# Performance work log

Hardware: AMD Instinct MI355X
Metric: run time of the kernel (lower is better)

The kernel has to match this reference:

```python
import jax, jax.numpy as jnp
import numpy as np
from jax import lax

WS = 7            # window size
DIM = 256         # out_dim
HEADS = 8
HD = DIM // HEADS # head dim = 32
HIDDEN = 4 * DIM  # mlp hidden = 1024
IN_DIM = 512
EPS = 1e-6

def _rel_pos_index(ws):
    coords = np.stack(np.meshgrid(np.arange(ws), np.arange(ws), indexing='ij'))
    cf = coords.reshape(2, -1)
    rc = (cf[:, :, None] - cf[:, None, :]).transpose(1, 2, 0)
    rc[:, :, 0] += ws - 1
    rc[:, :, 1] += ws - 1
    rc[:, :, 0] *= 2 * ws - 1
    return rc.sum(-1)  # (N, N)

RPI = jnp.asarray(_rel_pos_index(WS))  # (49, 49) int

def _layernorm(x, g, b):
    m = jnp.mean(x, axis=-1, keepdims=True)
    v = jnp.mean(jnp.square(x - m), axis=-1, keepdims=True)
    return (x - m) * lax.rsqrt(v + EPS) * g + b

def setup_inputs() -> dict:
    key = jax.random.key(0)
    ks = jax.random.split(key, 16)
    s = 0.02
    inp = {
        'x': jax.random.normal(ks[0], (8, IN_DIM, 48, 48), jnp.float32),
        'skip_feat': jax.random.normal(ks[1], (8, DIM, 96, 96), jnp.float32),
        # ConvTranspose2d(in, out, k=2, s=2): weight (in, out, 2, 2), bias (out,)
        'up_w': jax.random.normal(ks[2], (IN_DIM, DIM, 2, 2), jnp.float32) * s,
        'up_b': jnp.zeros((DIM,), jnp.float32),
        # skip_adapter Conv2d(out, out, 1, bias=False)
        'skip_w': jax.random.normal(ks[3], (DIM, DIM, 1, 1), jnp.float32) * s,
        'gamma1': jnp.ones((DIM,), jnp.float32),
        'beta1': jnp.zeros((DIM,), jnp.float32),
        'qkv_w': jax.random.normal(ks[4], (3 * DIM, DIM), jnp.float32) * s,
        'qkv_b': jnp.zeros((3 * DIM,), jnp.float32),
        'rpb_table': jax.random.normal(ks[5], ((2 * WS - 1) ** 2, HEADS), jnp.float32) * s,
        'proj_w': jax.random.normal(ks[6], (DIM, DIM), jnp.float32) * s,
        'proj_b': jnp.zeros((DIM,), jnp.float32),
        'gamma2': jnp.ones((DIM,), jnp.float32),
        'beta2': jnp.zeros((DIM,), jnp.float32),
        'mlp_w1': jax.random.normal(ks[7], (HIDDEN, DIM), jnp.float32) * s,
        'mlp_b1': jnp.zeros((HIDDEN,), jnp.float32),
        'mlp_w2': jax.random.normal(ks[8], (DIM, HIDDEN), jnp.float32) * s,
        'mlp_b2': jnp.zeros((DIM,), jnp.float32),
    }
    return inp

def _forward(x, skip_feat, up_w, up_b, skip_w, gamma1, beta1, qkv_w, qkv_b,
             rpb_table, proj_w, proj_b, gamma2, beta2, mlp_w1, mlp_b1, mlp_w2, mlp_b2):
    B = x.shape[0]
    # ConvTranspose2d k=2 s=2 p=0 == lhs-dilated conv with spatially flipped kernel
    y = lax.conv_general_dilated(
        x, jnp.flip(up_w, (2, 3)), window_strides=(1, 1),
        padding=((1, 1), (1, 1)), lhs_dilation=(2, 2),
        dimension_numbers=('NCHW', 'IOHW', 'NCHW')) + up_b[None, :, None, None]
    shortcut = y  # (B, C, Hup, Wup)
    # skip adapter (1x1 conv, no bias); shapes match so no interpolate/adhoc conv
    y = y + jnp.einsum('oi,bihw->bohw', skip_w[:, :, 0, 0], skip_feat)
    xh = jnp.transpose(y, (0, 2, 3, 1))  # (B, H, W, C)
    H, W, C = xh.shape[1], xh.shape[2], xh.shape[3]
    xn = _layernorm(xh, gamma1, beta1)
    pad_b = (WS - H % WS) % WS
    pad_r = (WS - W % WS) % WS
    xp = jnp.pad(xn, ((0, 0), (0, pad_b), (0, pad_r), (0, 0)))
    Hp, Wp = H + pad_b, W + pad_r
    N = WS * WS
    # window partition -> (B * nWh * nWw, N, C)
    win = xp.reshape(B, Hp // WS, WS, Wp // WS, WS, C)
    win = jnp.transpose(win, (0, 1, 3, 2, 4, 5)).reshape(-1, N, C)
    B_ = win.shape[0]
    # attention
    qkv = (win @ qkv_w.T + qkv_b).reshape(B_, N, 3, HEADS, HD)
    qkv = jnp.transpose(qkv, (2, 0, 3, 1, 4))  # (3, B_, h, N, hd)
    q, k, v = qkv[0], qkv[1], qkv[2]
    attn = jnp.einsum('bhnd,bhmd->bhnm', q * (HD ** -0.5), k)
    bias = rpb_table[RPI.reshape(-1)].reshape(N, N, HEADS)
    attn = attn + jnp.transpose(bias, (2, 0, 1))[None]  # (B_, h, N, N)
    attn = jax.nn.softmax(attn, axis=-1)
    o = jnp.einsum('bhnm,bhmd->bhnd', attn, v)
    o = jnp.transpose(o, (0, 2, 1, 3)).reshape(B_, N, C)
    o = o @ proj_w.T + proj_b
    # window reverse + crop
    o = o.reshape(B, Hp // WS, Wp // WS, WS, WS, C)
    o = jnp.transpose(o, (0, 1, 3, 2, 4, 5)).reshape(B, Hp, Wp, C)[:, :H, :W]
    x2 = jnp.transpose(shortcut, (0, 2, 3, 1)) + o
    # MLP
    h = jax.nn.gelu(_layernorm(x2, gamma2, beta2) @ mlp_w1.T + mlp_b1, approximate=False)
    x3 = x2 + (h @ mlp_w2.T + mlp_b2)
    return jnp.transpose(x3, (0, 3, 1, 2))  # (B, C, Hup, Wup)

def reference(x, skip_feat, up_w, up_b, skip_w, gamma1, beta1, qkv_w, qkv_b,
              rpb_table, proj_w, proj_b, gamma2, beta2, mlp_w1, mlp_b1, mlp_w2, mlp_b2):
    return _forward(x, skip_feat, up_w, up_b, skip_w, gamma1, beta1, qkv_w, qkv_b,
                    rpb_table, proj_w, proj_b, gamma2, beta2, mlp_w1, mlp_b1, mlp_w2, mlp_b2)
```

## Files before the change

kernel.cpp:

```cpp
#include <hip/hip_runtime.h>

typedef __attribute__((ext_vector_type(8))) short short8;
typedef __attribute__((ext_vector_type(4))) float f32x4;
typedef __attribute__((ext_vector_type(4))) unsigned short u16x4;
typedef unsigned short u16;
typedef unsigned int u32;

#define DEV static __device__ __forceinline__

DEV u16 f2b(float f) {
  u32 u = __builtin_bit_cast(u32, f);
  return (u16)((u + 0x7fffu + ((u >> 16) & 1u)) >> 16);
}
DEV float b2f(u16 h) {
  u32 u = ((u32)h) << 16;
  return __builtin_bit_cast(float, u);
}
DEV short8 ld8(const u16* p) { return *reinterpret_cast<const short8*>(p); }
DEV f32x4 mfma16(short8 a, short8 b, f32x4 c) {
  return __builtin_amdgcn_mfma_f32_16x16x32_bf16(a, b, c, 0, 0, 0);
}
DEV float wredsum(float v) {
#pragma unroll
  for (int off = 1; off < 64; off <<= 1) v += __shfl_xor(v, off);
  return v;
}

#define GLL(gp, lp) __builtin_amdgcn_global_load_lds( \
    (const __attribute__((address_space(1))) void*)(gp), \
    (__attribute__((address_space(3))) void*)(lp), 16, 0, 0)

#define WQKV   0
#define WPROJ  196608
#define WM1    262144
#define WM2    524288
#define WSKIP  786432
#define WUP    851968

#define OFF_BIAS 2752512u
#define OFF_SC   2883584u
#define OFF_OVR  40632320u
#define OFF_STAT (OFF_OVR + 52000000u)
#define OFF_PST  (OFF_OVR + 52600000u)
#define OFF_SGB  (OFF_OVR + 55000000u)
#define WS_NEED  96227328u

__global__ void k_sentinel(float* out) { out[threadIdx.x] = 31337.0f; }

__global__ __launch_bounds__(256) void k_prep(
    const float* qkv_w, const float* proj_w, const float* mlp_w1,
    const float* mlp_w2, const float* skip_w, const float* up_w,
    const float* rpb, const float* g1, const float* g2, u16* W, float* bias_g) {
  int i = blockIdx.x * 256 + threadIdx.x;
  if (i < 196608) { W[WQKV + i] = f2b(qkv_w[i] * g1[i & 255]); return; }
  i -= 196608;
  if (i < 65536) { W[WPROJ + i] = f2b(proj_w[i]); return; }
  i -= 65536;
  if (i < 262144) { W[WM1 + i] = f2b(mlp_w1[i] * g2[i & 255]); return; }
  i -= 262144;
  if (i < 262144) { W[WM2 + i] = f2b(mlp_w2[i]); return; }
  i -= 262144;
  if (i < 65536) { W[WSKIP + i] = f2b(skip_w[i]); return; }
  i -= 65536;
  if (i < 524288) {
    int ci = i & 511; int rest = i >> 9; int co = rest & 255; int kk = rest >> 8;
    W[WUP + i] = f2b(up_w[ci * 1024 + co * 4 + kk]);
    return;
  }
  i -= 524288;
  if (i < 32768) {
    int h = i >> 12, r = i & 4095, ii = r >> 6, j = r & 63;
    float v;
    if (j >= 49) v = -1e30f;
    else if (ii >= 49) v = 0.f;
    else {
      int d0 = (ii / 7 - j / 7) + 6, d1 = (ii % 7 - j % 7) + 6;
      v = rpb[(d0 * 13 + d1) * 8 + h];
    }
    bias_g[i] = v;
  }
}

__global__ __launch_bounds__(256) void k_fold(
    const float* mlp_w1, const float* qkv_w, const float* g1, const float* be1,
    const float* g2, const float* be2, float* sgb) {
  int wave = threadIdx.x >> 6, lane = threadIdx.x & 63;
  int id = blockIdx.x * 4 + wave;
  const float* wsrc;
  const float* vec;
  int out;
  if (id < 1024) { wsrc = mlp_w1 + (size_t)id * 256; vec = g2; out = id; }
  else if (id < 2048) { wsrc = mlp_w1 + (size_t)(id - 1024) * 256; vec = be2; out = id; }
  else { wsrc = qkv_w + (size_t)(id - 2048) * 256; vec = be1; out = 2816 + (id - 2048); }
  float s = 0.f;
#pragma unroll
  for (int j = 0; j < 4; j++) {
    int k = j * 64 + lane;
    s += vec[k] * wsrc[k];
  }
  s = wredsum(s);
  if (lane == 0) sgb[out] = s;
}

__global__ __launch_bounds__(256) void k_tr(const float* src, u16* dst, int C, int HW) {
  __shared__ float t[32][33];
  int hw0 = blockIdx.x * 32, c0 = blockIdx.y * 32, b = blockIdx.z;
  int tx = threadIdx.x & 31, ty = threadIdx.x >> 5;
  const float* s = src + (size_t)b * C * HW;
  u16* d = dst + (size_t)b * C * HW;
#pragma unroll
  for (int i = 0; i < 4; i++)
    t[ty + i * 8][tx] = s[(size_t)(c0 + ty + i * 8) * HW + hw0 + tx];
  __syncthreads();
#pragma unroll
  for (int i = 0; i < 4; i++)
    d[(size_t)(hw0 + ty + i * 8) * C + c0 + tx] = f2b(t[tx][ty + i * 8]);
}

__global__ __launch_bounds__(256) void k_tr_skip(const float* src, u16* dst) {
  __shared__ float t[32][33];
  int w0 = blockIdx.x * 32, c0 = blockIdx.y * 32;
  int z = blockIdx.z;
  int b = z / 96, h = z - b * 96;
  int tx = threadIdx.x & 31, ty = threadIdx.x >> 5;
  const float* s = src + (size_t)b * 256 * 9216 + (size_t)h * 96;
  u16* d = dst + (((size_t)b * 96 + h) * 96) * 256;
#pragma unroll
  for (int i = 0; i < 4; i++)
    t[ty + i * 8][tx] = s[(size_t)(c0 + ty + i * 8) * 9216 + w0 + tx];
  __syncthreads();
#pragma unroll
  for (int i = 0; i < 4; i++)
    d[(size_t)(w0 + ty + i * 8) * 256 + c0 + tx] = f2b(t[tx][ty + i * 8]);
}

__global__ __launch_bounds__(256) void k1g(
    const u16* W, const u16* xt, const float* up_b, u16* sc) {
  __shared__ __align__(16) u16 Ab[2][4096];
  __shared__ __align__(16) u16 Bb[2][4096];
  int tid = threadIdx.x;
  int lane = tid & 63, wave = tid >> 6;
  int m = lane & 15, gq = lane >> 4;
  int wr = wave >> 1, wc = wave & 1;
  int bm = blockIdx.x * 128, bn = blockIdx.y * 128;
  int kk = blockIdx.z, kh = kk >> 1, kw = kk & 1;
  const u16* Ag = xt + (size_t)bm * 512;
  const u16* Bg = W + WUP + (size_t)kk * 131072 + (size_t)bn * 512;
  f32x4 acc[4][4] = {};
#pragma unroll
  for (int c = 0; c < 2; c++) {
    int flat = (wave * 2 + c) * 512 + lane * 8;
    int r = flat >> 5, cc = flat & 31;
    GLL(Ag + (size_t)r * 512 + cc, &Ab[0][(wave * 2 + c) * 512]);
    GLL(Bg + (size_t)r * 512 + cc, &Bb[0][(wave * 2 + c) * 512]);
  }
  __syncthreads();
  int cur = 0;
  for (int ki = 0; ki < 16; ki++) {
    if (ki < 15) {
      int kkk = (ki + 1) * 32;
#pragma unroll
      for (int c = 0; c < 2; c++) {
        int flat = (wave * 2 + c) * 512 + lane * 8;
        int r = flat >> 5, cc = flat & 31;
        GLL(Ag + (size_t)r * 512 + kkk + cc, &Ab[cur ^ 1][(wave * 2 + c) * 512]);
        GLL(Bg + (size_t)r * 512 + kkk + cc, &Bb[cur ^ 1][(wave * 2 + c) * 512]);
      }
    }
    short8 aF[4], bF[4];
#pragma unroll
    for (int mt = 0; mt < 4; mt++)
      aF[mt] = ld8(&Ab[cur][(wr * 64 + mt * 16 + m) * 32 + gq * 8]);
#pragma unroll
    for (int nt = 0; nt < 4; nt++)
      bF[nt] = ld8(&Bb[cur][(wc * 64 + nt * 16 + m) * 32 + gq * 8]);
#pragma unroll
    for (int mt = 0; mt < 4; mt++)
#pragma unroll
      for (int nt = 0; nt < 4; nt++)
        acc[mt][nt] = mfma16(aF[mt], bF[nt], acc[mt][nt]);
    __syncthreads();
    cur ^= 1;
  }
  float ub[4];
#pragma unroll
  for (int nt = 0; nt < 4; nt++) ub[nt] = up_b[bn + wc * 64 + nt * 16 + m];
#pragma unroll
  for (int mt = 0; mt < 4; mt++)
#pragma unroll
    for (int rr = 0; rr < 4; rr++) {
      int t = bm + wr * 64 + mt * 16 + gq * 4 + rr;
      int b = t / 2304, rem = t - b * 2304;
      int ih = rem / 48, iw = rem - ih * 48;
      int h = 2 * ih + kh, w = 2 * iw + kw;
      size_t tok = ((size_t)b * 96 + h) * 96 + w;
#pragma unroll
      for (int nt = 0; nt < 4; nt++) {
        int ch = bn + wc * 64 + nt * 16 + m;
        sc[tok * 256 + ch] = f2b(acc[mt][nt][rr] + ub[nt]);
      }
    }
}

__global__ __launch_bounds__(256) void k2y(
    const u16* W, const u16* skt, const u16* sc, u16* ybuf, float* pstat) {
  __shared__ __align__(16) u16 Ab[2][4096];
  __shared__ __align__(16) u16 Bb[2][4096];
  int tid = threadIdx.x;
  int lane = tid & 63, wave = tid >> 6;
  int m = lane & 15, gq = lane >> 4;
  int wr = wave >> 1, wc = wave & 1;
  int bm = blockIdx.x * 128, bn = blockIdx.y * 128;
  const u16* Ag = skt + (size_t)bm * 256;
  const u16* Bg = W + WSKIP + (size_t)bn * 256;
  f32x4 acc[4][4] = {};
#pragma unroll
  for (int c = 0; c < 2; c++) {
    int flat = (wave * 2 + c) * 512 + lane * 8;
    int r = flat >> 5, cc = flat & 31;
    GLL(Ag + (size_t)r * 256 + cc, &Ab[0][(wave * 2 + c) * 512]);
    GLL(Bg + (size_t)r * 256 + cc, &Bb[0][(wave * 2 + c) * 512]);
  }
  __syncthreads();
  int cur = 0;
  for (int ki = 0; ki < 8; ki++) {
    if (ki < 7) {
      int kk = (ki + 1) * 32;
#pragma unroll
      for (int c = 0; c < 2; c++) {
        int flat = (wave * 2 + c) * 512 + lane * 8;
        int r = flat >> 5, cc = flat & 31;
        GLL(Ag + (size_t)r * 256 + kk + cc, &Ab[cur ^ 1][(wave * 2 + c) * 512]);
        GLL(Bg + (size_t)r * 256 + kk + cc, &Bb[cur ^ 1][(wave * 2 + c) * 512]);
      }
    }
    short8 aF[4], bF[4];
#pragma unroll
    for (int mt = 0; mt < 4; mt++)
      aF[mt] = ld8(&Ab[cur][(wr * 64 + mt * 16 + m) * 32 + gq * 8]);
#pragma unroll
    for (int nt = 0; nt < 4; nt++)
      bF[nt] = ld8(&Bb[cur][(wc * 64 + nt * 16 + m) * 32 + gq * 8]);
#pragma unroll
    for (int mt = 0; mt < 4; mt++)
#pragma unroll
      for (int nt = 0; nt < 4; nt++)
        acc[mt][nt] = mfma16(aF[mt], bF[nt], acc[mt][nt]);
    __syncthreads();
    cur ^= 1;
  }
#pragma unroll
  for (int mt = 0; mt < 4; mt++)
#pragma unroll
    for (int rr = 0; rr < 4; rr++) {
      int tok = bm + wr * 64 + mt * 16 + gq * 4 + rr;
      float s = 0.f, s2 = 0.f;
#pragma unroll
      for (int nt = 0; nt < 4; nt++) {
        int ch = bn + wc * 64 + nt * 16 + m;
        float y = acc[mt][nt][rr] + b2f(sc[(size_t)tok * 256 + ch]);
        ybuf[(size_t)tok * 256 + ch] = f2b(y);
        s += y; s2 += y * y;
      }
#pragma unroll
      for (int off = 1; off < 16; off <<= 1) {
        s += __shfl_xor(s, off);
        s2 += __shfl_xor(s2, off);
      }
      if (m == 0) {
        int pi = (tok * 4 + blockIdx.y * 2 + wc) * 2;
        pstat[pi] = s;
        pstat[pi + 1] = s2;
      }
    }
}

__global__ __launch_bounds__(256) void k_statfin(const float* pstat, float* stat) {
  int row = blockIdx.x * 256 + threadIdx.x;
  float s = 0.f, s2 = 0.f;
#pragma unroll
  for (int j = 0; j < 4; j++) {
    s += pstat[(row * 4 + j) * 2];
    s2 += pstat[(row * 4 + j) * 2 + 1];
  }
  float mean = s * 0.00390625f;
  float var = s2 * 0.00390625f - mean * mean;
  float r = rsqrtf(var + 1e-6f);
  stat[row * 2] = r;
  stat[row * 2 + 1] = r * mean;
}

__global__ __launch_bounds__(256) void k23(
    const u16* W, const u16* ybuf, const float* stat, const float* sgb,
    const float* qkv_b, const float* bias_g, u16* obr) {
  __shared__ __align__(16) u16 yl[49 * 264];
  __shared__ __align__(16) u16 pws[4][6144];
  int tid = threadIdx.x;
  int lane = tid & 63, wave = tid >> 6;
  int m = lane & 15, gq = lane >> 4, k0 = gq * 8;
  int blk = blockIdx.x;
  int bimg = blk / 196, wl = blk - bimg * 196;
  int wrow = wl / 14, wcol = wl - wrow * 14;
  int h0 = wrow * 7, w0 = wcol * 7;
  u16* prv = pws[wave];
#pragma unroll
  for (int t = 0; t < 8; t++) {
    u16x4 z = {};
    *reinterpret_cast<u16x4*>(&prv[t * 256 + lane * 4]) = z;
  }
  for (int it = 0; it < 7; it++) {
    int flat = it * 256 + tid;
    if (flat < 1568) {
      int row = flat >> 5, cc = (flat & 31) * 8;
      int hh = h0 + row / 7, ww = w0 + row % 7;
      short8 v = {};
      if (hh < 96 && ww < 96) {
        int ras = (bimg * 96 + hh) * 96 + ww;
        short8 raw = ld8(ybuf + (size_t)ras * 256 + cc);
        float rs = stat[ras * 2], rmu = stat[ras * 2 + 1];
#pragma unroll
        for (int q2 = 0; q2 < 8; q2++) {
          float zz = b2f(((const u16*)&raw)[q2]) * rs - rmu;
          ((u16*)&v)[q2] = f2b(zz);
        }
      }
      *reinterpret_cast<short8*>(&yl[row * 264 + cc]) = v;
    }
  }
  __syncthreads();
  const float scale = 0.1767766952966369f;
#pragma unroll
  for (int hp = 0; hp < 2; hp++) {
    int h = wave * 2 + hp;
    {
      const u16* bb0 = W + WQKV + (size_t)(h * 32 + m) * 256;
      const u16* bb1 = W + WQKV + (size_t)(h * 32 + 16 + m) * 256;
      const u16* bb2 = W + WQKV + (size_t)(256 + h * 32 + m) * 256;
      const u16* bb3 = W + WQKV + (size_t)(256 + h * 32 + 16 + m) * 256;
      f32x4 acc[4][4] = {};
#pragma unroll 4
      for (int ks = 0; ks < 8; ks++) {
        short8 a[4];
#pragma unroll
        for (int mt = 0; mt < 4; mt++) {
          int row = mt * 16 + m; if (row > 48) row = 48;
          a[mt] = ld8(&yl[row * 264 + ks * 32 + k0]);
        }
        short8 b0 = ld8(bb0 + ks * 32 + k0);
        short8 b1 = ld8(bb1 + ks * 32 + k0);
        short8 b2 = ld8(bb2 + ks * 32 + k0);
        short8 b3 = ld8(bb3 + ks * 32 + k0);
#pragma unroll
        for (int mt = 0; mt < 4; mt++) {
          acc[mt][0] = mfma16(a[mt], b0, acc[mt][0]);
          acc[mt][1] = mfma16(a[mt], b1, acc[mt][1]);
          acc[mt][2] = mfma16(a[mt], b2, acc[mt][2]);
          acc[mt][3] = mfma16(a[mt], b3, acc[mt][3]);
        }
      }
#pragma unroll
      for (int nt = 0; nt < 4; nt++) {
        int hd = (nt & 1) * 16 + m;
        int c = (nt >> 1) * 256 + h * 32 + hd;
        float qb_ = qkv_b[c];
        float sb1 = sgb[2816 + c];
        int base = (nt < 2) ? 2048 : 3616;
#pragma unroll
        for (int mt = 0; mt < 4; mt++)
#pragma unroll
          for (int rr = 0; rr < 4; rr++) {
            int row = mt * 16 + gq * 4 + rr;
            if (row >= 49) continue;
            int hh = h0 + row / 7, ww = w0 + row % 7;
            float vf = (hh < 96 && ww < 96) ? 1.f : 0.f;
            prv[base + row * 32 + hd] = f2b(acc[mt][nt][rr] + vf * sb1 + qb_);
          }
      }
    }
    {
      const u16* bb0 = W + WQKV + (size_t)(512 + h * 32 + m) * 256;
      const u16* bb1 = W + WQKV + (size_t)(512 + h * 32 + 16 + m) * 256;
      f32x4 vacc[4][2] = {};
#pragma unroll 4
      for (int ks = 0; ks < 8; ks++) {
        short8 a[4];
#pragma unroll
        for (int mt = 0; mt < 4; mt++) {
          int row = mt * 16 + m; if (row > 48) row = 48;
          a[mt] = ld8(&yl[row * 264 + ks * 32 + k0]);
        }
        short8 b0 = ld8(bb0 + ks * 32 + k0);
        short8 b1 = ld8(bb1 + ks * 32 + k0);
#pragma unroll
        for (int mt = 0; mt < 4; mt++) {
          vacc[mt][0] = mfma16(a[mt], b0, vacc[mt][0]);
          vacc[mt][1] = mfma16(a[mt], b1, vacc[mt][1]);
        }
      }
      int vsw = (m & 7) * 8;
#pragma unroll
      for (int nv = 0; nv < 2; nv++) {
        int hd = nv * 16 + m;
        int c = 512 + h * 32 + hd;
        float qb_ = qkv_b[c];
        float sb1 = sgb[2816 + c];
#pragma unroll
        for (int mt = 0; mt < 4; mt++)
#pragma unroll
          for (int rr = 0; rr < 4; rr++) {
            int row = mt * 16 + gq * 4 + rr;
            if (row >= 49) continue;
            int hh = h0 + row / 7, ww = w0 + row % 7;
            float vf = (hh < 96 && ww < 96) ? 1.f : 0.f;
            prv[hd * 64 + (row ^ vsw)] = f2b(vacc[mt][nv][rr] + vf * sb1 + qb_);
          }
      }
    }
    short8 aq[4], bk[4];
#pragma unroll
    for (int mt = 0; mt < 4; mt++) { int i = mt * 16 + m; if (i > 48) i = 48; aq[mt] = ld8(&prv[2048 + i * 32 + k0]); }
#pragma unroll
    for (int nt = 0; nt < 4; nt++) { int j = nt * 16 + m; if (j > 48) j = 48; bk[nt] = ld8(&prv[3616 + j * 32 + k0]); }
    f32x4 s[4][4] = {};
#pragma unroll
    for (int mt = 0; mt < 4; mt++)
#pragma unroll
      for (int nt = 0; nt < 4; nt++)
        s[mt][nt] = mfma16(aq[mt], bk[nt], s[mt][nt]);
    const float* BI = bias_g + h * 4096;
    float rsum[4][4];
#pragma unroll
    for (int mt = 0; mt < 4; mt++)
#pragma unroll
      for (int rr = 0; rr < 4; rr++) {
        int i = mt * 16 + gq * 4 + rr;
        float sv[4];
        float mx = -1e38f;
#pragma unroll
        for (int nt = 0; nt < 4; nt++) {
          sv[nt] = s[mt][nt][rr] * scale + BI[i * 64 + nt * 16 + m];
          mx = fmaxf(mx, sv[nt]);
        }
        mx = fmaxf(mx, __shfl_xor(mx, 1));
        mx = fmaxf(mx, __shfl_xor(mx, 2));
        mx = fmaxf(mx, __shfl_xor(mx, 4));
        mx = fmaxf(mx, __shfl_xor(mx, 8));
        float sum = 0.f;
#pragma unroll
        for (int nt = 0; nt < 4; nt++) { sv[nt] = __expf(sv[nt] - mx); sum += sv[nt]; }
        sum += __shfl_xor(sum, 1);
        sum += __shfl_xor(sum, 2);
        sum += __shfl_xor(sum, 4);
        sum += __shfl_xor(sum, 8);
        rsum[mt][rr] = sum;
        int isw = (i & 7) * 8;
#pragma unroll
        for (int nt = 0; nt < 4; nt++) {
          int j = nt * 16 + m;
          prv[2048 + i * 64 + (j ^ isw)] = f2b(sv[nt]);
        }
      }
    f32x4 o[4][2] = {};
#pragma unroll
    for (int ks = 0; ks < 2; ks++) {
      short8 bv[2];
#pragma unroll
      for (int nt = 0; nt < 2; nt++) {
        int hd = nt * 16 + m;
        bv[nt] = ld8(&prv[hd * 64 + ((ks * 32 + k0) ^ ((hd & 7) * 8))]);
      }
#pragma unroll
      for (int mt = 0; mt < 4; mt++) {
        int i = mt * 16 + m;
        short8 ap = *reinterpret_cast<const short8*>(
            &prv[2048 + i * 64 + ((ks * 32 + k0) ^ ((i & 7) * 8))]);
#pragma unroll
        for (int nt = 0; nt < 2; nt++)
          o[mt][nt] = mfma16(ap, bv[nt], o[mt][nt]);
      }
    }
#pragma unroll
    for (int mt = 0; mt < 4; mt++)
#pragma unroll
      for (int rr = 0; rr < 4; rr++) {
        int i = mt * 16 + gq * 4 + rr;
        if (i >= 49) continue;
        int hh = h0 + i / 7, ww = w0 + i % 7;
        if (hh >= 96 || ww >= 96) continue;
        size_t ras = ((size_t)bimg * 96 + hh) * 96 + ww;
        float rinv = 1.f / rsum[mt][rr];
#pragma unroll
        for (int nt = 0; nt < 2; nt++) {
          int c = h * 32 + nt * 16 + m;
          obr[ras * 256 + c] = f2b(o[mt][nt][rr] * rinv);
        }
      }
  }
}

__global__ __launch_bounds__(256) void k4r(
    const u16* W, const u16* obr, const float* proj_b, u16* sc, float* pstat) {
  __shared__ __align__(16) u16 Ab[2][4096];
  __shared__ __align__(16) u16 Bb[2][4096];
  int tid = threadIdx.x;
  int lane = tid & 63, wave = tid >> 6;
  int m = lane & 15, gq = lane >> 4;
  int wr = wave >> 1, wc = wave & 1;
  int bm = blockIdx.x * 128, bn = blockIdx.y * 128;
  const u16* Ag = obr + (size_t)bm * 256;
  const u16* Bg = W + WPROJ + (size_t)bn * 256;
  f32x4 acc[4][4] = {};
#pragma unroll
  for (int c = 0; c < 2; c++) {
    int flat = (wave * 2 + c) * 512 + lane * 8;
    int r = flat >> 5, cc = flat & 31;
    GLL(Ag + (size_t)r * 256 + cc, &Ab[0][(wave * 2 + c) * 512]);
    GLL(Bg + (size_t)r * 256 + cc, &Bb[0][(wave * 2 + c) * 512]);
  }
  __syncthreads();
  int cur = 0;
  for (int ki = 0; ki < 8; ki++) {
    if (ki < 7) {
      int kk = (ki + 1) * 32;
#pragma unroll
      for (int c = 0; c < 2; c++) {
        int flat = (wave * 2 + c) * 512 + lane * 8;
        int r = flat >> 5, cc = flat & 31;
        GLL(Ag + (size_t)r * 256 + kk + cc, &Ab[cur ^ 1][(wave * 2 + c) * 512]);
        GLL(Bg + (size_t)r * 256 + kk + cc, &Bb[cur ^ 1][(wave * 2 + c) * 512]);
      }
    }
    short8 aF[4], bF[4];
#pragma unroll
    for (int mt = 0; mt < 4; mt++)
      aF[mt] = ld8(&Ab[cur][(wr * 64 + mt * 16 + m) * 32 + gq * 8]);
#pragma unroll
    for (int nt = 0; nt < 4; nt++)
      bF[nt] = ld8(&Bb[cur][(wc * 64 + nt * 16 + m) * 32 + gq * 8]);
#pragma unroll
    for (int mt = 0; mt < 4; mt++)
#pragma unroll
      for (int nt = 0; nt < 4; nt++)
        acc[mt][nt] = mfma16(aF[mt], bF[nt], acc[mt][nt]);
    __syncthreads();
    cur ^= 1;
  }
#pragma unroll
  for (int mt = 0; mt < 4; mt++)
#pragma unroll
    for (int rr = 0; rr < 4; rr++) {
      int tok = bm + wr * 64 + mt * 16 + gq * 4 + rr;
      float s = 0.f, s2 = 0.f;
#pragma unroll
      for (int nt = 0; nt < 4; nt++) {
        int ch = bn + wc * 64 + nt * 16 + m;
        float v = acc[mt][nt][rr] + proj_b[ch] + b2f(sc[(size_t)tok * 256 + ch]);
        sc[(size_t)tok * 256 + ch] = f2b(v);
        s += v; s2 += v * v;
      }
#pragma unroll
      for (int off = 1; off < 16; off <<= 1) {
        s += __shfl_xor(s, off);
        s2 += __shfl_xor(s2, off);
      }
      if (m == 0) {
        int pi = (tok * 4 + blockIdx.y * 2 + wc) * 2;
        pstat[pi] = s;
        pstat[pi + 1] = s2;
      }
    }
}

__global__ __launch_bounds__(256) void k56(
    const u16* W, const u16* x2, const float* stat, const float* sgb,
    const float* mb1, const float* mb2, float* out) {
  __shared__ __align__(16) u16 XA[64 * 264];
  __shared__ __align__(16) u16 HC[64 * 136];
  int tid = threadIdx.x;
  int lane = tid & 63, wave = tid >> 6;
  int m = lane & 15, gq = lane >> 4, k0 = gq * 8;
  int tok0 = blockIdx.x * 64;
#pragma unroll
  for (int it = 0; it < 8; it++) {
    int flat = it * 2048 + tid * 8;
    int row = flat >> 8, col = flat & 255;
    *reinterpret_cast<short8*>(&XA[row * 264 + col]) =
        ld8(x2 + (size_t)(tok0 + row) * 256 + col);
  }
  float rsv[4][4], rmuv[4][4];
#pragma unroll
  for (int mt = 0; mt < 4; mt++)
#pragma unroll
    for (int rr = 0; rr < 4; rr++) {
      int tok = tok0 + mt * 16 + gq * 4 + rr;
      rsv[mt][rr] = stat[tok * 2];
      rmuv[mt][rr] = stat[tok * 2 + 1];
    }
  __syncthreads();
  f32x4 acc2[4][4] = {};
  for (int c = 0; c < 8; c++) {
    const u16* B1a = W + WM1 + (size_t)(c * 128 + wave * 32 + m) * 256;
    const u16* B1b = W + WM1 + (size_t)(c * 128 + wave * 32 + 16 + m) * 256;
    f32x4 acc1[4][2] = {};
#pragma unroll
    for (int ks = 0; ks < 8; ks++) {
      short8 a[4];
#pragma unroll
      for (int mt = 0; mt < 4; mt++)
        a[mt] = ld8(&XA[(mt * 16 + m) * 264 + ks * 32 + k0]);
      short8 b0 = ld8(B1a + ks * 32 + k0);
      short8 b1 = ld8(B1b + ks * 32 + k0);
#pragma unroll
      for (int mt = 0; mt < 4; mt++) {
        acc1[mt][0] = mfma16(a[mt], b0, acc1[mt][0]);
        acc1[mt][1] = mfma16(a[mt], b1, acc1[mt][1]);
      }
    }
#pragma unroll
    for (int nt = 0; nt < 2; nt++) {
      int col = wave * 32 + nt * 16 + m;
      int ch = c * 128 + col;
      float sg = sgb[ch], sb = sgb[1024 + ch], b1v = mb1[ch];
#pragma unroll
      for (int mt = 0; mt < 4; mt++)
#pragma unroll
        for (int rr = 0; rr < 4; rr++) {
          int tl = mt * 16 + gq * 4 + rr;
          float v = rsv[mt][rr] * acc1[mt][nt][rr] - rmuv[mt][rr] * sg + sb + b1v;
          float u = v * v;
          float y = v * __builtin_fmaf(0.07135481627f, u, 1.595769122f);
          float g = v / (1.f + __expf(-y));
          HC[tl * 136 + col] = f2b(g);
        }
    }
    __syncthreads();
#pragma unroll
    for (int ks = 0; ks < 4; ks++) {
      short8 a2[4];
#pragma unroll
      for (int mt = 0; mt < 4; mt++)
        a2[mt] = ld8(&HC[(mt * 16 + m) * 136 + ks * 32 + k0]);
      short8 bF[4];
#pragma unroll
      for (int nt = 0; nt < 4; nt++) {
        int ch = wave * 64 + nt * 16 + m;
        bF[nt] = ld8(W + WM2 + (size_t)ch * 1024 + c * 128 + ks * 32 + k0);
      }
#pragma unroll
      for (int mt = 0; mt < 4; mt++)
#pragma unroll
        for (int nt = 0; nt < 4; nt++)
          acc2[mt][nt] = mfma16(a2[mt], bF[nt], acc2[mt][nt]);
    }
    __syncthreads();
  }
#pragma unroll
  for (int nt = 0; nt < 4; nt++) {
    int ch = wave * 64 + nt * 16 + m;
    float bias = mb2[ch];
#pragma unroll
    for (int mt = 0; mt < 4; mt++)
#pragma unroll
      for (int rr = 0; rr < 4; rr++) {
        int tl = mt * 16 + gq * 4 + rr;
        acc2[mt][nt][rr] += bias + b2f(XA[tl * 264 + ch]);
      }
  }
  __syncthreads();
  float* ot = (float*)XA;
  int tg = tok0;
  int bimg = tg / 9216, hw0 = tg % 9216;
#pragma unroll
  for (int half = 0; half < 2; half++) {
    if ((wave >> 1) == half) {
#pragma unroll
      for (int nt = 0; nt < 4; nt++) {
        int jj = (wave & 1) * 64 + nt * 16 + m;
#pragma unroll
        for (int mt = 0; mt < 4; mt++)
#pragma unroll
          for (int rr = 0; rr < 4; rr++) {
            int tl = mt * 16 + gq * 4 + rr;
            ot[jj * 66 + tl] = acc2[mt][nt][rr];
          }
      }
    }
    __syncthreads();
    for (int it = 0; it < 32; it++) {
      int flat = it * 256 + tid;
      int j = flat >> 6, t = flat & 63;
      out[((size_t)bimg * 256 + half * 128 + j) * 9216 + hw0 + t] = ot[j * 66 + t];
    }
    __syncthreads();
  }
}

extern "C" void kernel_launch(void* const* d_in, const int* in_sizes, int n_in,
                              void* d_out, int out_size, void* d_ws, size_t ws_size,
                              hipStream_t stream) {
  const float* x      = (const float*)d_in[0];
  const float* skipf  = (const float*)d_in[1];
  const float* up_w   = (const float*)d_in[2];
  const float* up_b   = (const float*)d_in[3];
  const float* skip_w = (const float*)d_in[4];
  const float* g1     = (const float*)d_in[5];
  const float* be1    = (const float*)d_in[6];
  const float* qkv_w  = (const float*)d_in[7];
  const float* qkv_b  = (const float*)d_in[8];
  const float* rpb    = (const float*)d_in[9];
  const float* proj_w = (const float*)d_in[10];
  const float* proj_b = (const float*)d_in[11];
  const float* g2     = (const float*)d_in[12];
  const float* be2    = (const float*)d_in[13];
  const float* m_w1   = (const float*)d_in[14];
  const float* m_b1   = (const float*)d_in[15];
  const float* m_w2   = (const float*)d_in[16];
  const float* m_b2   = (const float*)d_in[17];
  if (ws_size < WS_NEED) {
    k_sentinel<<<1, 256, 0, stream>>>((float*)d_out);
    return;
  }
  char* ws = (char*)d_ws;
  u16*   W    = (u16*)ws;
  float* bias = (float*)(ws + OFF_BIAS);
  u16*   sc   = (u16*)(ws + OFF_SC);
  u16*   xt   = (u16*)(ws + OFF_OVR);
  u16*   skt  = (u16*)(ws + OFF_OVR);
  float* stat = (float*)(ws + OFF_STAT);
  float* pst  = (float*)(ws + OFF_PST);
  float* sgb  = (float*)(ws + OFF_SGB);
  u16*   ybuf = (u16*)d_out;
  u16*   obr  = (u16*)((char*)d_out + 37748736u);

  k_prep<<<5504, 256, 0, stream>>>(qkv_w, proj_w, m_w1, m_w2, skip_w, up_w, rpb,
                                   g1, g2, W, bias);
  k_fold<<<704, 256, 0, stream>>>(m_w1, qkv_w, g1, be1, g2, be2, sgb);
  k_tr<<<dim3(72, 16, 8), 256, 0, stream>>>(x, xt, 512, 2304);
  k1g<<<dim3(144, 2, 4), 256, 0, stream>>>(W, xt, up_b, sc);
  k_tr_skip<<<dim3(3, 8, 768), 256, 0, stream>>>(skipf, skt);
  k2y<<<dim3(576, 2), 256, 0, stream>>>(W, skt, sc, ybuf, pst);
  k_statfin<<<288, 256, 0, stream>>>(pst, stat);
  k23<<<1568, 256, 0, stream>>>(W, ybuf, stat, sgb, qkv_b, bias, obr);
  k4r<<<dim3(576, 2), 256, 0, stream>>>(W, obr, proj_b, sc, pst);
  k_statfin<<<288, 256, 0, stream>>>(pst, stat);
  k56<<<1152, 256, 0, stream>>>(W, sc, stat, sgb, m_b1, m_b2, (float*)d_out);
}
```

Before: 575.7 us.

## Fuse output projection, residual and LayerNorm stats into MLP kernel

The attention output projection, bias, residual add and per-token LayerNorm statistics are now computed inside the MLP kernel for each 64-token tile, with x2 kept in shared memory. This removes the separate projection kernel, one stat-finalisation launch, and the global write and re-read of x2 and the partial stats. The obr buffer moves from the output region into the workspace overlay. The cost is that projection weights are read straight from global memory per block rather than tiled through shared memory, and the fused kernel does more work per block.

```diff
diff --git a/kernel.cpp b/kernel.cpp
--- a/kernel.cpp
+++ b/kernel.cpp
@@ -498,82 +498,9 @@
   }
 }
 
-__global__ __launch_bounds__(256) void k4r(
-    const u16* W, const u16* obr, const float* proj_b, u16* sc, float* pstat) {
-  __shared__ __align__(16) u16 Ab[2][4096];
-  __shared__ __align__(16) u16 Bb[2][4096];
-  int tid = threadIdx.x;
-  int lane = tid & 63, wave = tid >> 6;
-  int m = lane & 15, gq = lane >> 4;
-  int wr = wave >> 1, wc = wave & 1;
-  int bm = blockIdx.x * 128, bn = blockIdx.y * 128;
-  const u16* Ag = obr + (size_t)bm * 256;
-  const u16* Bg = W + WPROJ + (size_t)bn * 256;
-  f32x4 acc[4][4] = {};
-#pragma unroll
-  for (int c = 0; c < 2; c++) {
-    int flat = (wave * 2 + c) * 512 + lane * 8;
-    int r = flat >> 5, cc = flat & 31;
-    GLL(Ag + (size_t)r * 256 + cc, &Ab[0][(wave * 2 + c) * 512]);
-    GLL(Bg + (size_t)r * 256 + cc, &Bb[0][(wave * 2 + c) * 512]);
-  }
-  __syncthreads();
-  int cur = 0;
-  for (int ki = 0; ki < 8; ki++) {
-    if (ki < 7) {
-      int kk = (ki + 1) * 32;
-#pragma unroll
-      for (int c = 0; c < 2; c++) {
-        int flat = (wave * 2 + c) * 512 + lane * 8;
-        int r = flat >> 5, cc = flat & 31;
-        GLL(Ag + (size_t)r * 256 + kk + cc, &Ab[cur ^ 1][(wave * 2 + c) * 512]);
-        GLL(Bg + (size_t)r * 256 + kk + cc, &Bb[cur ^ 1][(wave * 2 + c) * 512]);
-      }
-    }
-    short8 aF[4], bF[4];
-#pragma unroll
-    for (int mt = 0; mt < 4; mt++)
-      aF[mt] = ld8(&Ab[cur][(wr * 64 + mt * 16 + m) * 32 + gq * 8]);
-#pragma unroll
-    for (int nt = 0; nt < 4; nt++)
-      bF[nt] = ld8(&Bb[cur][(wc * 64 + nt * 16 + m) * 32 + gq * 8]);
-#pragma unroll
-    for (int mt = 0; mt < 4; mt++)
-#pragma unroll
-      for (int nt = 0; nt < 4; nt++)
-        acc[mt][nt] = mfma16(aF[mt], bF[nt], acc[mt][nt]);
-    __syncthreads();
-    cur ^= 1;
-  }
-#pragma unroll
-  for (int mt = 0; mt < 4; mt++)
-#pragma unroll
-    for (int rr = 0; rr < 4; rr++) {
-      int tok = bm + wr * 64 + mt * 16 + gq * 4 + rr;
-      float s = 0.f, s2 = 0.f;
-#pragma unroll
-      for (int nt = 0; nt < 4; nt++) {
-        int ch = bn + wc * 64 + nt * 16 + m;
-        float v = acc[mt][nt][rr] + proj_b[ch] + b2f(sc[(size_t)tok * 256 + ch]);
-        sc[(size_t)tok * 256 + ch] = f2b(v);
-        s += v; s2 += v * v;
-      }
-#pragma unroll
-      for (int off = 1; off < 16; off <<= 1) {
-        s += __shfl_xor(s, off);
-        s2 += __shfl_xor(s2, off);
-      }
-      if (m == 0) {
-        int pi = (tok * 4 + blockIdx.y * 2 + wc) * 2;
-        pstat[pi] = s;
-        pstat[pi + 1] = s2;
-      }
-    }
-}
-
-__global__ __launch_bounds__(256) void k56(
-    const u16* W, const u16* x2, const float* stat, const float* sgb,
-    const float* mb1, const float* mb2, float* out) {
+__global__ __launch_bounds__(256) void k456(
+    const u16* W, const u16* obr, const u16* sc, const float* proj_b,
+    const float* sgb, const float* mb1, const float* mb2, float* out) {
   __shared__ __align__(16) u16 XA[64 * 264];
   __shared__ __align__(16) u16 HC[64 * 136];
   int tid = threadIdx.x;
@@ -585,16 +512,83 @@
     int flat = it * 2048 + tid * 8;
     int row = flat >> 8, col = flat & 255;
     *reinterpret_cast<short8*>(&XA[row * 264 + col]) =
-        ld8(x2 + (size_t)(tok0 + row) * 256 + col);
-  }
+        ld8(obr + (size_t)(tok0 + row) * 256 + col);
+  }
+  __syncthreads();
+  f32x4 accp[4][4] = {};
+  {
+    const u16* b0p = W + WPROJ + (size_t)(wave * 64 + m) * 256;
+    const u16* b1p = W + WPROJ + (size_t)(wave * 64 + 16 + m) * 256;
+    const u16* b2p = W + WPROJ + (size_t)(wave * 64 + 32 + m) * 256;
+    const u16* b3p = W + WPROJ + (size_t)(wave * 64 + 48 + m) * 256;
+#pragma unroll
+    for (int ks = 0; ks < 8; ks++) {
+      short8 a[4];
+#pragma unroll
+      for (int mt = 0; mt < 4; mt++)
+        a[mt] = ld8(&XA[(mt * 16 + m) * 264 + ks * 32 + k0]);
+      short8 b0 = ld8(b0p + ks * 32 + k0);
+      short8 b1 = ld8(b1p + ks * 32 + k0);
+      short8 b2 = ld8(b2p + ks * 32 + k0);
+      short8 b3 = ld8(b3p + ks * 32 + k0);
+#pragma unroll
+      for (int mt = 0; mt < 4; mt++) {
+        accp[mt][0] = mfma16(a[mt], b0, accp[mt][0]);
+        accp[mt][1] = mfma16(a[mt], b1, accp[mt][1]);
+        accp[mt][2] = mfma16(a[mt], b2, accp[mt][2]);
+        accp[mt][3] = mfma16(a[mt], b3, accp[mt][3]);
+      }
+    }
+  }
+  __syncthreads();
+  float* pst_l = (float*)HC;
+  {
+    float pb[4];
+#pragma unroll
+    for (int nt = 0; nt < 4; nt++) pb[nt] = proj_b[wave * 64 + nt * 16 + m];
+#pragma unroll
+    for (int mt = 0; mt < 4; mt++)
+#pragma unroll
+      for (int rr = 0; rr < 4; rr++) {
+        int tl = mt * 16 + gq * 4 + rr;
+        size_t tok = tok0 + tl;
+        float s = 0.f, s2 = 0.f;
+#pragma unroll
+        for (int nt = 0; nt < 4; nt++) {
+          int ch = wave * 64 + nt * 16 + m;
+          float v = accp[mt][nt][rr] + pb[nt] + b2f(sc[tok * 256 + ch]);
+          XA[tl * 264 + ch] = f2b(v);
+          s += v; s2 += v * v;
+        }
+#pragma unroll
+        for (int off = 1; off < 16; off <<= 1) {
+          s += __shfl_xor(s, off);
+          s2 += __shfl_xor(s2, off);
+        }
+        if (m == 0) {
+          pst_l[tl * 8 + wave * 2] = s;
+          pst_l[tl * 8 + wave * 2 + 1] = s2;
+        }
+      }
+  }
+  __syncthreads();
   float rsv[4][4], rmuv[4][4];
 #pragma unroll
   for (int mt = 0; mt < 4; mt++)
 #pragma unroll
     for (int rr = 0; rr < 4; rr++) {
-      int tok = tok0 + mt * 16 + gq * 4 + rr;
-      rsv[mt][rr] = stat[tok * 2];
-      rmuv[mt][rr] = stat[tok * 2 + 1];
+      int tl = mt * 16 + gq * 4 + rr;
+      float s = 0.f, s2 = 0.f;
+#pragma unroll
+      for (int j = 0; j < 4; j++) {
+        s += pst_l[tl * 8 + j * 2];
+        s2 += pst_l[tl * 8 + j * 2 + 1];
+      }
+      float mean = s * 0.00390625f;
+      float var = s2 * 0.00390625f - mean * mean;
+      float r = rsqrtf(var + 1e-6f);
+      rsv[mt][rr] = r;
+      rmuv[mt][rr] = r * mean;
     }
   __syncthreads();
   f32x4 acc2[4][4] = {};
@@ -726,11 +720,11 @@
   u16*   sc   = (u16*)(ws + OFF_SC);
   u16*   xt   = (u16*)(ws + OFF_OVR);
   u16*   skt  = (u16*)(ws + OFF_OVR);
+  u16*   obr  = (u16*)(ws + OFF_OVR);
   float* stat = (float*)(ws + OFF_STAT);
   float* pst  = (float*)(ws + OFF_PST);
   float* sgb  = (float*)(ws + OFF_SGB);
   u16*   ybuf = (u16*)d_out;
-  u16*   obr  = (u16*)((char*)d_out + 37748736u);
 
   k_prep<<<5504, 256, 0, stream>>>(qkv_w, proj_w, m_w1, m_w2, skip_w, up_w, rpb,
                                    g1, g2, W, bias);
@@ -741,7 +735,6 @@
   k2y<<<dim3(576, 2), 256, 0, stream>>>(W, skt, sc, ybuf, pst);
   k_statfin<<<288, 256, 0, stream>>>(pst, stat);
   k23<<<1568, 256, 0, stream>>>(W, ybuf, stat, sgb, qkv_b, bias, obr);
-  k4r<<<dim3(576, 2), 256, 0, stream>>>(W, obr, proj_b, sc, pst);
-  k_statfin<<<288, 256, 0, stream>>>(pst, stat);
-  k56<<<1152, 256, 0, stream>>>(W, sc, stat, sgb, m_b1, m_b2, (float*)d_out);
-}
+  k456<<<1152, 256, 0, stream>>>(W, obr, sc, proj_b, sgb, m_b1, m_b2,
+                                 (float*)d_out);
+}
```

New measurement: 581.2 us. No clear change (+1.0%).
